# Optimization experiments

Hardware: AMD Instinct MI355X
Metric: run time of the kernel (lower is better)

Reference implementation:

```python
import jax, jax.numpy as jnp
import numpy as np

NUM_HEADS = 16


def rotate_half(x):
    x1 = x[..., ::2]
    x2 = x[..., 1::2]
    return jnp.concatenate((-x2, x1), axis=-1)


def rope_sin_cos(seq_len, head_dim, dtype):
    inv_freq = 1.0 / (10000.0 ** (jnp.arange(0, head_dim, 2, dtype=jnp.float32) / head_dim))
    t = jnp.arange(seq_len, dtype=jnp.float32)
    freqs = jnp.einsum('i,j->ij', t, inv_freq)          # [S, D/2]
    emb = jnp.concatenate((freqs, freqs), axis=-1)      # [S, D]
    return jnp.sin(emb).astype(dtype), jnp.cos(emb).astype(dtype)


def setup_inputs() -> dict:
    key = jax.random.key(0)
    B, S, E = 2, 2048, 2048
    ks = jax.random.split(key, 5)
    scale = 1.0 / np.sqrt(E)
    return {
        'x': jax.random.normal(ks[0], (B, S, E), dtype=jnp.float32),
        'mask': jnp.ones((B, S), dtype=jnp.int32),
        'Wq': jax.random.normal(ks[1], (E, E), dtype=jnp.float32) * scale,
        'bq': jnp.zeros((E,), dtype=jnp.float32),
        'Wk': jax.random.normal(ks[2], (E, E), dtype=jnp.float32) * scale,
        'bk': jnp.zeros((E,), dtype=jnp.float32),
        'Wv': jax.random.normal(ks[3], (E, E), dtype=jnp.float32) * scale,
        'bv': jnp.zeros((E,), dtype=jnp.float32),
        'Wo': jax.random.normal(ks[4], (E, E), dtype=jnp.float32) * scale,
        'bo': jnp.zeros((E,), dtype=jnp.float32),
    }


def reference(x, mask, Wq, bq, Wk, bk, Wv, bv, Wo, bo):
    B, S, E = x.shape
    H = NUM_HEADS
    D = E // H
    q = (x @ Wq + bq).reshape(B, S, H, D).transpose(0, 2, 1, 3)  # [B,H,S,D]
    k = (x @ Wk + bk).reshape(B, S, H, D).transpose(0, 2, 1, 3)
    v = (x @ Wv + bv).reshape(B, S, H, D).transpose(0, 2, 1, 3)

    sin, cos = rope_sin_cos(S, D, q.dtype)  # [S,D]
    sin = sin[None, None]                    # [1,1,S,D]
    cos = cos[None, None]
    q = q * cos + rotate_half(q) * sin
    k = k * cos + rotate_half(k) * sin

    scores = jnp.einsum('bhqd,bhkd->bhqk', q, k) / jnp.sqrt(jnp.asarray(D, q.dtype))
    scores = jnp.where(mask[:, None, None, :] == 0, -jnp.inf, scores)
    probs = jax.nn.softmax(scores, axis=-1)
    attn = jnp.einsum('bhqk,bhkd->bhqd', probs, v)       # [B,H,S,D]
    attn = attn.transpose(0, 2, 1, 3).reshape(B, S, E)
    return attn @ Wo + bo
```

## Files before the change

### kernel.cpp

```cpp
#include <hip/hip_runtime.h>
#include <hip/hip_bf16.h>
#include <cmath>

typedef unsigned short u16;
typedef unsigned int   u32;

using v4f    = __attribute__((ext_vector_type(4)))  float;
using f32x16 = __attribute__((ext_vector_type(16))) float;
using s8v    = __attribute__((ext_vector_type(8)))  short;
using u32x2  = __attribute__((ext_vector_type(2)))  unsigned int;

union Frag { uint4 u; s8v s; };

__device__ __forceinline__ u16 f2bf(float f){
  u32 u = __float_as_uint(f);
  u32 r = u + 0x7fffu + ((u >> 16) & 1u);
  return (u16)(r >> 16);
}
__device__ __forceinline__ float bf2f(u16 h){ return __uint_as_float(((u32)h) << 16); }

__device__ __forceinline__ u32 cvtpk(float a, float b){
  u32 r;
  asm("v_cvt_pk_bf16_f32 %0, %1, %2" : "=v"(r) : "v"(a), "v"(b));
  return r;
}

__device__ __forceinline__ void async16(const void* g, void* l){
  __builtin_amdgcn_global_load_lds((__attribute__((address_space(1))) void*)g,
                                   (__attribute__((address_space(3))) void*)l, 16, 0, 0);
}

__global__ __launch_bounds__(256) void prep_kernel(
    const float* __restrict__ x, u16* __restrict__ xb,
    const float* __restrict__ W0, const float* __restrict__ W1,
    const float* __restrict__ W2, const float* __restrict__ W3,
    u16* __restrict__ T0, u16* __restrict__ T1, u16* __restrict__ T2, u16* __restrict__ T3,
    float2* __restrict__ tab){
  __shared__ float tile[64][65];
  const int bid = blockIdx.x;
  if (bid < 8192){
    size_t i = ((size_t)bid * 256 + threadIdx.x) * 4;
    float4 v = *(const float4*)(x + i);
    uint2 o;
    o.x = (u32)f2bf(v.x) | ((u32)f2bf(v.y) << 16);
    o.y = (u32)f2bf(v.z) | ((u32)f2bf(v.w) << 16);
    *(uint2*)(xb + i) = o;
    return;
  }
  if (bid >= 12288){
    const int idx = (bid - 12288)*256 + threadIdx.x;
    const int s = idx >> 6, j = idx & 63;
    float invf = exp2f(-(float)j * 0.20762050593045952f);
    float sn, cs;
    sincosf((float)s * invf, &sn, &cs);
    tab[idx] = make_float2(sn, cs);
    return;
  }
  const int t4 = bid - 8192;
  const int z  = t4 >> 10;
  const float* W = (z==0)?W0:(z==1)?W1:(z==2)?W2:W3;
  u16*         T = (z==0)?T0:(z==1)?T1:(z==2)?T2:T3;
  const int k0 = ((t4 & 1023) >> 5)*64, n0 = (t4 & 31)*64;
  const int t  = threadIdx.x;
  const int rr = t >> 4, c4 = (t & 15) * 4;
  #pragma unroll
  for (int i=0;i<4;i++){
    int k = rr + i*16;
    float4 v = *(const float4*)(W + (size_t)(k0+k)*2048 + n0 + c4);
    tile[k][c4+0]=v.x; tile[k][c4+1]=v.y; tile[k][c4+2]=v.z; tile[k][c4+3]=v.w;
  }
  __syncthreads();
  #pragma unroll
  for (int i=0;i<4;i++){
    int n = rr + i*16;
    uint2 o;
    o.x = (u32)f2bf(tile[c4+0][n]) | ((u32)f2bf(tile[c4+1][n])<<16);
    o.y = (u32)f2bf(tile[c4+2][n]) | ((u32)f2bf(tile[c4+3][n])<<16);
    *(uint2*)(T + (size_t)(n0+n)*2048 + k0 + c4) = o;
  }
}

template<int MODE>
__device__ __forceinline__ void gemm_tile(const u16* __restrict__ A, const u16* __restrict__ BT,
                                          const float* __restrict__ bias, void* __restrict__ Cout,
                                          int m0, int n0, u16* sm, const float2* __restrict__ tab){
  constexpr int K = 2048;
  u16* Asl = sm;
  u16* Bsl = sm + 8192;
  const int tid  = threadIdx.x;
  const int w    = tid >> 6;
  const int lane = tid & 63;
  const int r    = lane & 15, q = lane >> 4;
  const int wm   = (w >> 1) * 64, wn = (w & 1) * 64;

  v4f acc[4][4];
  #pragma unroll
  for (int i=0;i<4;i++)
    #pragma unroll
    for (int j=0;j<4;j++) acc[i][j] = (v4f)0.f;

  const int srow = w*32 + (lane>>3);
  const int sblk = (lane&7) ^ ((lane>>3)&7);
  const u16* Ag = A  + (size_t)(m0+srow)*K + sblk*8;
  const u16* Bg = BT + (size_t)(n0+srow)*K + sblk*8;
  u16* Als = Asl + (w*32)*64;
  u16* Bls = Bsl + (w*32)*64;

  for (int kk = 0; kk < K; kk += 64) {
    #pragma unroll
    for (int i=0;i<4;i++){
      async16(Ag + (size_t)i*8*K + kk, Als + i*512);
      async16(Bg + (size_t)i*8*K + kk, Bls + i*512);
    }
    __syncthreads();
    #pragma unroll
    for (int ks=0; ks<2; ++ks) {
      s8v af[4], bfr[4];
      #pragma unroll
      for (int i=0;i<4;i++){
        int rho = wm + i*16 + r;
        int p = (ks*4 + q) ^ (r&7);
        Frag t; t.u = *(const uint4*)(Asl + rho*64 + p*8); af[i] = t.s;
      }
      #pragma unroll
      for (int j=0;j<4;j++){
        int rho = wn + j*16 + r;
        int p = (ks*4 + q) ^ (r&7);
        Frag t; t.u = *(const uint4*)(Bsl + rho*64 + p*8); bfr[j] = t.s;
      }
      #pragma unroll
      for (int i=0;i<4;i++)
        #pragma unroll
        for (int j=0;j<4;j++)
          acc[i][j] = __builtin_amdgcn_mfma_f32_16x16x32_bf16(af[i], bfr[j], acc[i][j], 0, 0, 0);
    }
    __syncthreads();
  }

  float bv[4];
  #pragma unroll
  for (int j=0;j<4;j++) bv[j] = bias[n0 + wn + j*16 + r];

  if constexpr (MODE != 3){
    #pragma unroll
    for (int i=0;i<4;i++){
      #pragma unroll
      for (int j=0;j<4;j++){
        const int gn = n0 + wn + j*16 + r;
        #pragma unroll
        for (int rr2=0; rr2<4; ++rr2){
          const int gm = m0 + wm + i*16 + q*4 + rr2;
          float val = acc[i][j][rr2] + bv[j];
          if (MODE == 0) ((u16*)Cout)[(size_t)gm*2048 + gn] = f2bf(val);
          else           ((float*)Cout)[(size_t)gm*2048 + gn] = val;
        }
      }
    }
  } else {
    #pragma unroll
    for (int i=0;i<4;i++)
      #pragma unroll
      for (int j=0;j<4;j++){
        const int col = wn + j*16 + r;
        #pragma unroll
        for (int rr2=0; rr2<4; ++rr2)
          sm[(wm + i*16 + q*4 + rr2)*128 + col] = f2bf(acc[i][j][rr2] + bv[j]);
      }
    __syncthreads();
    for (int rr=0; rr<32; ++rr){
      const int row = w*32 + rr;
      const int s = (m0 + row) & 2047;
      float2 sc2 = tab[s*64 + lane];
      const u16* tr = sm + row*128;
      float x_j   = bf2f(tr[lane]);
      float x_j64 = bf2f(tr[64 + lane]);
      float x_2j  = bf2f(tr[2*lane]);
      float x_2j1 = bf2f(tr[2*lane + 1]);
      u16* gp = (u16*)Cout + (size_t)(m0 + row)*2048 + n0;
      gp[lane]      = f2bf(x_j  * sc2.y - x_2j1 * sc2.x);
      gp[64 + lane] = f2bf(x_j64 * sc2.y + x_2j  * sc2.x);
    }
  }
}

__global__ __launch_bounds__(256) void gemm_qkv_kernel(
    const u16* __restrict__ A,
    const u16* __restrict__ WqT, const u16* __restrict__ WkT, const u16* __restrict__ WvT,
    const float* __restrict__ bq, const float* __restrict__ bk, const float* __restrict__ bv,
    u16* __restrict__ Qb, u16* __restrict__ Kb, u16* __restrict__ Vb,
    const float2* __restrict__ tab){
  __shared__ u16 sm[16384];
  const int bx = blockIdx.x, by = blockIdx.y;
  const int mat = bx >> 4;
  const u16*   BT   = (mat==0)?WqT:(mat==1)?WkT:WvT;
  const float* bias = (mat==0)?bq :(mat==1)?bk :bv;
  u16*         Cout = (mat==0)?Qb :(mat==1)?Kb :Vb;
  if (mat < 2) gemm_tile<3>(A, BT, bias, Cout, by*128, (bx & 15)*128, sm, tab);
  else         gemm_tile<0>(A, BT, bias, Cout, by*128, (bx & 15)*128, sm, tab);
}

__global__ __launch_bounds__(256) void gemm_wo_kernel(const u16* __restrict__ A,
                                                      const u16* __restrict__ WoT,
                                                      const float* __restrict__ bias,
                                                      float* __restrict__ out){
  __shared__ u16 sm[16384];
  gemm_tile<1>(A, WoT, bias, out, blockIdx.y*128, blockIdx.x*128, sm, nullptr);
}

__global__ __launch_bounds__(256) void tv_kernel(const u16* __restrict__ V, u16* __restrict__ VT){
  __shared__ u16 t[64*72];
  const int tb = blockIdx.x;
  const int s0 = (tb & 31)*64;
  const int d0 = ((tb >> 5) & 1)*64;
  const int bh = tb >> 6;
  const int b = bh >> 4, h = bh & 15;
  const size_t obase = ((size_t)bh*128 + d0)*2048 + s0;
  const int tid = threadIdx.x;
  #pragma unroll
  for (int i=0;i<2;i++){
    int c = tid + i*256;
    int sl = c >> 3, dc = (c & 7) * 8;
    *(uint4*)(t + sl*72 + dc) =
      *(const uint4*)(V + ((size_t)(b*2048 + s0 + sl))*2048 + h*128 + d0 + dc);
  }
  __syncthreads();
  #pragma unroll
  for (int i=0;i<2;i++){
    int c = tid + i*256;
    int dl = c >> 3, sc4 = (c & 7) * 8;
    u16 tmp[8];
    #pragma unroll
    for (int j=0;j<8;j++) tmp[j] = t[(sc4+j)*72 + dl];
    *(uint4*)(VT + obase + (size_t)dl*2048 + sc4) = *(const uint4*)tmp;
  }
}

__global__ __launch_bounds__(128,2) void attn_kernel(const u16* __restrict__ Q,
                                                     const u16* __restrict__ K,
                                                     const u16* __restrict__ VT,
                                                     const int* __restrict__ mask,
                                                     u16* __restrict__ Out){
  constexpr int S = 2048;
  constexpr float SL2 = 0.08838834764831845f * 1.4426950408889634f;
  __shared__ u16 smem[16384];

  const int tid = threadIdx.x, w = tid >> 6, lane = tid & 63;
  const int qc = lane & 31;
  const int h  = lane >> 5;
  const int l7 = lane & 7;
  const int hh = blockIdx.y, b = blockIdx.z;
  const int q0 = blockIdx.x * 64;
  const size_t rowb = (size_t)b * 2048;
  const size_t bhD  = ((size_t)(b*16 + hh)) * 128;

  s8v qf[8];
  {
    const u16* qp = Q + (rowb + q0 + w*32 + qc)*2048 + hh*128 + h*8;
    #pragma unroll
    for (int t=0;t<8;t++){ Frag f; f.u = *(const uint4*)(qp + t*16); qf[t] = f.s; }
  }

  f32x16 accO[4];
  #pragma unroll
  for (int d=0; d<4; d++) accO[d] = (f32x16)0.f;
  float lsum = 0.f;

  const int sr4 = lane >> 4, sp16 = lane & 15;
  const int vr8 = lane >> 3, vp8 = lane & 7;

  for (int it=0; it<32; ++it){
    const int key0 = it*64;
    int mv = mask[b*S + key0 + lane];
    #pragma unroll
    for (int i=0;i<8;i++){
      int R = w*32 + i*4;
      int ob = sp16 ^ ((R&7) + sr4);
      async16(K + (rowb + key0 + R + sr4)*2048 + hh*128 + ob*8, smem + R*128);
    }
    #pragma unroll
    for (int i=0;i<8;i++){
      int R = w*64 + i*8;
      int ob = vp8 ^ vr8;
      async16(VT + (bhD + R + vr8)*2048 + key0 + ob*8, smem + 8192 + R*64);
    }
    __syncthreads();
    unsigned long long bm = __ballot(mv != 0);
    const u16* Ks = smem;
    const u16* Vs = smem + 8192;

    #pragma unroll
    for (int nb=0; nb<2; ++nb){
      f32x16 sc = (f32x16)0.f;
      __builtin_amdgcn_s_setprio(1);
      #pragma unroll
      for (int t=0;t<8;t++){
        Frag kf; kf.u = *(const uint4*)(Ks + (nb*32 + qc)*128 + (((2*t + h) ^ l7)*8));
        sc = __builtin_amdgcn_mfma_f32_32x32x16_bf16(kf.s, qf[t], sc, 0, 0, 0);
      }
      __builtin_amdgcn_s_setprio(0);
      float p[16];
      #pragma unroll
      for (int m=0; m<16; ++m) p[m] = exp2f(sc[m] * SL2);
      if (bm != ~0ull){
        #pragma unroll
        for (int m=0; m<16; ++m){
          int bit = nb*32 + (m&3) + 8*(m>>2) + 4*h;
          if (!((bm >> bit) & 1ull)) p[m] = 0.f;
        }
      }
      #pragma unroll
      for (int m=0; m<16; ++m) lsum += p[m];

      #pragma unroll
      for (int g=0; g<2; ++g){
        u32 a0 = cvtpk(p[8*g+0], p[8*g+1]);
        u32 a1 = cvtpk(p[8*g+2], p[8*g+3]);
        u32 a2 = cvtpk(p[8*g+4], p[8*g+5]);
        u32 a3 = cvtpk(p[8*g+6], p[8*g+7]);
        u32x2 r0 = __builtin_amdgcn_permlane32_swap(a0, a2, false, false);
        u32x2 r1 = __builtin_amdgcn_permlane32_swap(a1, a3, false, false);
        Frag pf; pf.u = make_uint4(r0[0], r1[0], r0[1], r1[1]);
        const int T = nb*2 + g;
        __builtin_amdgcn_s_setprio(1);
        #pragma unroll
        for (int d=0; d<4; ++d){
          Frag vf; vf.u = *(const uint4*)(Vs + (d*32 + qc)*64 + (((2*T + h) ^ l7)*8));
          accO[d] = __builtin_amdgcn_mfma_f32_32x32x16_bf16(vf.s, pf.s, accO[d], 0, 0, 0);
        }
        __builtin_amdgcn_s_setprio(0);
      }
    }
    __syncthreads();
  }

  float sall = lsum + __shfl_xor(lsum, 32, 64);
  float invv = (sall > 0.f) ? 1.f/sall : 0.f;
  u16* orow = Out + (rowb + q0 + w*32 + qc)*2048 + hh*128;
  #pragma unroll
  for (int d=0; d<4; ++d){
    #pragma unroll
    for (int g2=0; g2<4; ++g2){
      uint2 o;
      o.x = cvtpk(accO[d][g2*4+0] * invv, accO[d][g2*4+1] * invv);
      o.y = cvtpk(accO[d][g2*4+2] * invv, accO[d][g2*4+3] * invv);
      *(uint2*)(orow + d*32 + g2*8 + 4*h) = o;
    }
  }
}

extern "C" void kernel_launch(void* const* d_in, const int* in_sizes, int n_in,
                              void* d_out, int out_size, void* d_ws, size_t ws_size,
                              hipStream_t stream) {
  (void)in_sizes; (void)n_in; (void)out_size; (void)ws_size;
  const float* x    = (const float*)d_in[0];
  const int*   mask = (const int*)d_in[1];
  const float* Wq   = (const float*)d_in[2];
  const float* bq   = (const float*)d_in[3];
  const float* Wk   = (const float*)d_in[4];
  const float* bk   = (const float*)d_in[5];
  const float* Wv   = (const float*)d_in[6];
  const float* bv   = (const float*)d_in[7];
  const float* Wo   = (const float*)d_in[8];
  const float* bo   = (const float*)d_in[9];

  u16* xbf = (u16*)d_ws;
  u16* WqT = xbf + 8388608;
  u16* WkT = WqT + 4194304;
  u16* WvT = WkT + 4194304;
  u16* WoT = WvT + 4194304;
  u16* Qb  = WoT + 4194304;
  u16* Kb  = Qb + 8388608;
  u16* Vb  = Kb + 8388608;
  u16* VTb = Vb + 8388608;
  u16* Ab  = VTb + 8388608;
  float2* tab = (float2*)Ab;

  prep_kernel<<<12800, 256, 0, stream>>>(x, xbf, Wq, Wk, Wv, Wo, WqT, WkT, WvT, WoT, tab);
  gemm_qkv_kernel<<<dim3(48,32), 256, 0, stream>>>(xbf, WqT, WkT, WvT, bq, bk, bv, Qb, Kb, Vb, tab);
  tv_kernel<<<2048, 256, 0, stream>>>(Vb, VTb);
  attn_kernel<<<dim3(32,16,2), 128, 0, stream>>>(Qb, Kb, VTb, mask, Ab);
  gemm_wo_kernel<<<dim3(16,32), 256, 0, stream>>>(Ab, WoT, bo, (float*)d_out);
}
```

Baseline: 421.8 us.

## Process two 32-row query tiles per wave in attention to reuse K/V loads

Each attention wave now handles 64 query rows as two 32-row sub-tiles, so every K and V fragment read from shared memory feeds two MFMAs. The grid's query dimension is halved to match, which halves global K/V tile loads per head. This raises register use (two score tiles, two sets of output accumulators, two Q fragment sets) under launch_bounds(128,2) and may risk spills. It also cuts the block count to 512. The RoPE epilogue loop in the QKV GEMM is also partially unrolled.

```diff
diff --git a/kernel.cpp b/kernel.cpp
--- a/kernel.cpp
+++ b/kernel.cpp
@@ -167,6 +167,7 @@
           sm[(wm + i*16 + q*4 + rr2)*128 + col] = f2bf(acc[i][j][rr2] + bv[j]);
       }
     __syncthreads();
+    #pragma unroll 8
     for (int rr=0; rr<32; ++rr){
       const int row = w*32 + rr;
       const int s = (m0 + row) & 2047;
@@ -249,21 +250,25 @@
   const int h  = lane >> 5;
   const int l7 = lane & 7;
   const int hh = blockIdx.y, b = blockIdx.z;
-  const int q0 = blockIdx.x * 64;
+  const int q0 = blockIdx.x * 128;
   const size_t rowb = (size_t)b * 2048;
   const size_t bhD  = ((size_t)(b*16 + hh)) * 128;
 
-  s8v qf[8];
+  s8v qfA[8], qfB[8];
   {
-    const u16* qp = Q + (rowb + q0 + w*32 + qc)*2048 + hh*128 + h*8;
-    #pragma unroll
-    for (int t=0;t<8;t++){ Frag f; f.u = *(const uint4*)(qp + t*16); qf[t] = f.s; }
-  }
-
-  f32x16 accO[4];
-  #pragma unroll
-  for (int d=0; d<4; d++) accO[d] = (f32x16)0.f;
-  float lsum = 0.f;
+    const u16* qpA = Q + (rowb + q0 + w*64 + qc)*2048 + hh*128 + h*8;
+    const u16* qpB = qpA + (size_t)32*2048;
+    #pragma unroll
+    for (int t=0;t<8;t++){
+      Frag fa; fa.u = *(const uint4*)(qpA + t*16); qfA[t] = fa.s;
+      Frag fb; fb.u = *(const uint4*)(qpB + t*16); qfB[t] = fb.s;
+    }
+  }
+
+  f32x16 accA[4], accB[4];
+  #pragma unroll
+  for (int d=0; d<4; d++){ accA[d] = (f32x16)0.f; accB[d] = (f32x16)0.f; }
+  float lsumA = 0.f, lsumB = 0.f;
 
   const int sr4 = lane >> 4, sp16 = lane & 15;
   const int vr8 = lane >> 3, vp8 = lane & 7;
@@ -290,42 +295,51 @@
 
     #pragma unroll
     for (int nb=0; nb<2; ++nb){
-      f32x16 sc = (f32x16)0.f;
+      f32x16 scA = (f32x16)0.f, scB = (f32x16)0.f;
       __builtin_amdgcn_s_setprio(1);
       #pragma unroll
       for (int t=0;t<8;t++){
         Frag kf; kf.u = *(const uint4*)(Ks + (nb*32 + qc)*128 + (((2*t + h) ^ l7)*8));
-        sc = __builtin_amdgcn_mfma_f32_32x32x16_bf16(kf.s, qf[t], sc, 0, 0, 0);
+        scA = __builtin_amdgcn_mfma_f32_32x32x16_bf16(kf.s, qfA[t], scA, 0, 0, 0);
+        scB = __builtin_amdgcn_mfma_f32_32x32x16_bf16(kf.s, qfB[t], scB, 0, 0, 0);
       }
       __builtin_amdgcn_s_setprio(0);
-      float p[16];
-      #pragma unroll
-      for (int m=0; m<16; ++m) p[m] = exp2f(sc[m] * SL2);
+      float pA[16], pB[16];
+      #pragma unroll
+      for (int m=0; m<16; ++m){ pA[m] = exp2f(scA[m] * SL2); pB[m] = exp2f(scB[m] * SL2); }
       if (bm != ~0ull){
         #pragma unroll
         for (int m=0; m<16; ++m){
           int bit = nb*32 + (m&3) + 8*(m>>2) + 4*h;
-          if (!((bm >> bit) & 1ull)) p[m] = 0.f;
+          if (!((bm >> bit) & 1ull)){ pA[m] = 0.f; pB[m] = 0.f; }
         }
       }
       #pragma unroll
-      for (int m=0; m<16; ++m) lsum += p[m];
+      for (int m=0; m<16; ++m){ lsumA += pA[m]; lsumB += pB[m]; }
 
       #pragma unroll
       for (int g=0; g<2; ++g){
-        u32 a0 = cvtpk(p[8*g+0], p[8*g+1]);
-        u32 a1 = cvtpk(p[8*g+2], p[8*g+3]);
-        u32 a2 = cvtpk(p[8*g+4], p[8*g+5]);
-        u32 a3 = cvtpk(p[8*g+6], p[8*g+7]);
+        u32 a0 = cvtpk(pA[8*g+0], pA[8*g+1]);
+        u32 a1 = cvtpk(pA[8*g+2], pA[8*g+3]);
+        u32 a2 = cvtpk(pA[8*g+4], pA[8*g+5]);
+        u32 a3 = cvtpk(pA[8*g+6], pA[8*g+7]);
         u32x2 r0 = __builtin_amdgcn_permlane32_swap(a0, a2, false, false);
         u32x2 r1 = __builtin_amdgcn_permlane32_swap(a1, a3, false, false);
-        Frag pf; pf.u = make_uint4(r0[0], r1[0], r0[1], r1[1]);
+        Frag pfA; pfA.u = make_uint4(r0[0], r1[0], r0[1], r1[1]);
+        u32 b0 = cvtpk(pB[8*g+0], pB[8*g+1]);
+        u32 b1 = cvtpk(pB[8*g+2], pB[8*g+3]);
+        u32 b2 = cvtpk(pB[8*g+4], pB[8*g+5]);
+        u32 b3 = cvtpk(pB[8*g+6], pB[8*g+7]);
+        u32x2 s0 = __builtin_amdgcn_permlane32_swap(b0, b2, false, false);
+        u32x2 s1 = __builtin_amdgcn_permlane32_swap(b1, b3, false, false);
+        Frag pfB; pfB.u = make_uint4(s0[0], s1[0], s0[1], s1[1]);
         const int T = nb*2 + g;
         __builtin_amdgcn_s_setprio(1);
         #pragma unroll
         for (int d=0; d<4; ++d){
           Frag vf; vf.u = *(const uint4*)(Vs + (d*32 + qc)*64 + (((2*T + h) ^ l7)*8));
-          accO[d] = __builtin_amdgcn_mfma_f32_32x32x16_bf16(vf.s, pf.s, accO[d], 0, 0, 0);
+          accA[d] = __builtin_amdgcn_mfma_f32_32x32x16_bf16(vf.s, pfA.s, accA[d], 0, 0, 0);
+          accB[d] = __builtin_amdgcn_mfma_f32_32x32x16_bf16(vf.s, pfB.s, accB[d], 0, 0, 0);
         }
         __builtin_amdgcn_s_setprio(0);
       }
@@ -333,17 +347,23 @@
     __syncthreads();
   }
 
-  float sall = lsum + __shfl_xor(lsum, 32, 64);
-  float invv = (sall > 0.f) ? 1.f/sall : 0.f;
-  u16* orow = Out + (rowb + q0 + w*32 + qc)*2048 + hh*128;
+  float sallA = lsumA + __shfl_xor(lsumA, 32, 64);
+  float sallB = lsumB + __shfl_xor(lsumB, 32, 64);
+  float invA = (sallA > 0.f) ? 1.f/sallA : 0.f;
+  float invB = (sallB > 0.f) ? 1.f/sallB : 0.f;
+  u16* orowA = Out + (rowb + q0 + w*64 + qc)*2048 + hh*128;
+  u16* orowB = orowA + (size_t)32*2048;
   #pragma unroll
   for (int d=0; d<4; ++d){
     #pragma unroll
     for (int g2=0; g2<4; ++g2){
-      uint2 o;
-      o.x = cvtpk(accO[d][g2*4+0] * invv, accO[d][g2*4+1] * invv);
-      o.y = cvtpk(accO[d][g2*4+2] * invv, accO[d][g2*4+3] * invv);
-      *(uint2*)(orow + d*32 + g2*8 + 4*h) = o;
+      uint2 oa, ob2;
+      oa.x  = cvtpk(accA[d][g2*4+0] * invA, accA[d][g2*4+1] * invA);
+      oa.y  = cvtpk(accA[d][g2*4+2] * invA, accA[d][g2*4+3] * invA);
+      ob2.x = cvtpk(accB[d][g2*4+0] * invB, accB[d][g2*4+1] * invB);
+      ob2.y = cvtpk(accB[d][g2*4+2] * invB, accB[d][g2*4+3] * invB);
+      *(uint2*)(orowA + d*32 + g2*8 + 4*h) = oa;
+      *(uint2*)(orowB + d*32 + g2*8 + 4*h) = ob2;
     }
   }
 }
@@ -378,6 +398,6 @@
   prep_kernel<<<12800, 256, 0, stream>>>(x, xbf, Wq, Wk, Wv, Wo, WqT, WkT, WvT, WoT, tab);
   gemm_qkv_kernel<<<dim3(48,32), 256, 0, stream>>>(xbf, WqT, WkT, WvT, bq, bk, bv, Qb, Kb, Vb, tab);
   tv_kernel<<<2048, 256, 0, stream>>>(Vb, VTb);
-  attn_kernel<<<dim3(32,16,2), 128, 0, stream>>>(Qb, Kb, VTb, mask, Ab);
+  attn_kernel<<<dim3(16,16,2), 128, 0, stream>>>(Qb, Kb, VTb, mask, Ab);
   gemm_wo_kernel<<<dim3(16,32), 256, 0, stream>>>(Ab, WoT, bo, (float*)d_out);
 }
```

Result: slower. 577.2 us (+36.8%).
